# Optimization experiments

Measured on AMD Instinct MI355X. Metric: run time of the kernel, lower is better.

## Reference

```python
import jax, jax.numpy as jnp
import numpy as np

D_MODEL = 1024
N_HEADS = 16
D_K = D_MODEL // N_HEADS
THETA = 10000.0
B, S = 4, 2048


def _rope(x, positions):
    # x: [B, H, S, D_K]; positions: [S] int
    half = D_K // 2
    inv_freq = THETA ** (-jnp.arange(0, half, dtype=jnp.float32) * 2.0 / D_K)  # [half]
    ang = positions.astype(jnp.float32)[:, None] * inv_freq[None, :]  # [S, half]
    cos = jnp.cos(ang)[None, None, :, :]
    sin = jnp.sin(ang)[None, None, :, :]
    x_even = x[..., 0::2]
    x_odd = x[..., 1::2]
    out_even = x_even * cos - x_odd * sin
    out_odd = x_even * sin + x_odd * cos
    # interleave back to original layout
    out = jnp.stack([out_even, out_odd], axis=-1).reshape(x.shape)
    return out


def setup_inputs() -> dict:
    key = jax.random.key(0)
    ks = jax.random.split(key, 5)
    scale = 1.0 / np.sqrt(D_MODEL)
    return {
        "x": jax.random.normal(ks[0], (B, S, D_MODEL), dtype=jnp.float32),
        "token_positions": jnp.arange(S, dtype=jnp.int64 if jax.config.jax_enable_x64 else jnp.int32),
        "Wq": jax.random.normal(ks[1], (D_MODEL, D_MODEL), dtype=jnp.float32) * scale,
        "Wk": jax.random.normal(ks[2], (D_MODEL, D_MODEL), dtype=jnp.float32) * scale,
        "Wv": jax.random.normal(ks[3], (D_MODEL, D_MODEL), dtype=jnp.float32) * scale,
        "Wo": jax.random.normal(ks[4], (D_MODEL, D_MODEL), dtype=jnp.float32) * scale,
    }


def reference(x, token_positions, Wq, Wk, Wv, Wo):
    bsz, seq_len, _ = x.shape
    # projections (Linear_Transform: y = x @ W^T, no bias)
    def proj(W):
        h = jnp.einsum("bsd,ed->bse", x, W)
        return h.reshape(bsz, seq_len, N_HEADS, D_K).transpose(0, 2, 1, 3)  # [B,H,S,Dk]
    Q = proj(Wq)
    K = proj(Wk)
    V = proj(Wv)
    Q = _rope(Q, token_positions)
    K = _rope(K, token_positions)
    # scaled dot product attention with causal mask
    scores = jnp.einsum("bhqd,bhkd->bhqk", Q, K) / jnp.sqrt(jnp.float32(D_K))
    causal = jnp.tril(jnp.ones((seq_len, seq_len), dtype=bool))  # [S,S]
    scores = jnp.where(causal[None, None, :, :], scores, -jnp.inf)
    attn = jax.nn.softmax(scores, axis=-1)
    out = jnp.einsum("bhqk,bhkd->bhqd", attn, V)
    out = out.transpose(0, 2, 1, 3).reshape(bsz, seq_len, D_MODEL)
    return jnp.einsum("bsd,ed->bse", out, Wo)
```

## Files before the change

### kernel.cpp

```cpp
#include <hip/hip_runtime.h>
#include <hip/hip_bf16.h>
#include <cstdint>
#include <cstddef>

typedef __attribute__((ext_vector_type(4))) float f32x4;
typedef __attribute__((ext_vector_type(8))) short bf16x8;
typedef unsigned int u32;
typedef unsigned short u16;


__device__ __forceinline__ u16 f2bf(float x) {
  u32 u = __builtin_bit_cast(u32, x);
  u += 0x7fffu + ((u >> 16) & 1u);
  return (u16)(u >> 16);
}

__device__ __forceinline__ u32 cvt_pk_bf16(float lo, float hi) {
  u32 r;
  asm("v_cvt_pk_bf16_f32 %0, %1, %2" : "=v"(r) : "v"(lo), "v"(hi));
  return r;
}

__device__ __forceinline__ void gl_lds16(const void* g, void* l) {
  __builtin_amdgcn_global_load_lds(
      (const __attribute__((address_space(1))) u32*)(uintptr_t)g,
      (__attribute__((address_space(3))) u32*)(u32)(uintptr_t)l,
      16, 0, 0);
}

#define MFMA16(a, b, c) __builtin_amdgcn_mfma_f32_16x16x32_bf16((a), (b), (c), 0, 0, 0)


__global__ void cast_all_k(const float* __restrict__ x, const float* __restrict__ wq,
                           const float* __restrict__ wk, const float* __restrict__ wv,
                           const float* __restrict__ wo, u16* __restrict__ xb,
                           u16* __restrict__ wqb, u16* __restrict__ wkb,
                           u16* __restrict__ wvb, u16* __restrict__ wob) {
  int blk = blockIdx.x;
  const float* s; u16* d; int i;
  if (blk < 8192)       { s = x;  d = xb;  i = blk * 256; }
  else if (blk < 9216)  { s = wq; d = wqb; i = (blk - 8192) * 256; }
  else if (blk < 10240) { s = wk; d = wkb; i = (blk - 9216) * 256; }
  else if (blk < 11264) { s = wv; d = wvb; i = (blk - 10240) * 256; }
  else                  { s = wo; d = wob; i = (blk - 11264) * 256; }
  i += threadIdx.x;
  const float4 v = reinterpret_cast<const float4*>(s)[i];
  uint2 o;
  o.x = cvt_pk_bf16(v.x, v.y);
  o.y = cvt_pk_bf16(v.z, v.w);
  reinterpret_cast<uint2*>(d)[i] = o;
}


__global__ void rope_table_k(const int* __restrict__ pos, float2* __restrict__ cs) {
  int idx = blockIdx.x * 256 + threadIdx.x;
  int s = idx >> 5, i = idx & 31;
  float inv = powf(10000.0f, -(float)i * (1.0f / 32.0f));
  float ang = (float)pos[s] * inv;
  cs[idx] = float2{cosf(ang), sinf(ang)};
}


__global__ __launch_bounds__(256, 2)
void gemm_qkv(const u16* __restrict__ A, const u16* __restrict__ B,
              const float2* __restrict__ cs, u16* __restrict__ Qr,
              u16* __restrict__ Kr, u16* __restrict__ Vt, float qscale) {
  const int K = 1024;
  __shared__ u16 a_lds[2][128 * 32];
  __shared__ u16 b_lds[2][128 * 32];
  const int tid = threadIdx.x;
  const int l = tid & 63;
  const int w = tid >> 6;
  const int wm = w >> 1, wn = w & 1;
  const int bm = blockIdx.y, bn = blockIdx.x;

  const u16* Ab = A + (size_t)bm * 128 * K;
  const u16* Bb = B + (size_t)bn * 128 * K;

  auto stage = [&](int bq, int k0) {
#pragma unroll
    for (int half = 0; half < 2; ++half) {
      int t = half * 256 + tid;
      int row = t >> 2, slot = t & 3;
      int sp = slot ^ ((row >> 1) & 3);
      gl_lds16(Ab + (size_t)row * K + k0 + sp * 8, &a_lds[bq][t * 8]);
      gl_lds16(Bb + (size_t)row * K + k0 + sp * 8, &b_lds[bq][t * 8]);
    }
  };

  const f32x4 fz = {0.f, 0.f, 0.f, 0.f};
  f32x4 acc[4][4];
#pragma unroll
  for (int mi = 0; mi < 4; ++mi)
#pragma unroll
    for (int ni = 0; ni < 4; ++ni) acc[mi][ni] = fz;

  const int nk = K >> 5;
  stage(0, 0);
  int buf = 0;
  for (int kt = 0; kt < nk; ++kt) {
    __syncthreads();
    if (kt + 1 < nk) stage(buf ^ 1, (kt + 1) * 32);
    bf16x8 af[4], bf[4];
#pragma unroll
    for (int mi = 0; mi < 4; ++mi) {
      int row = wm * 64 + mi * 16 + (l & 15);
      int sp = (l >> 4) ^ ((row >> 1) & 3);
      af[mi] = *(const bf16x8*)&a_lds[buf][row * 32 + sp * 8];
    }
#pragma unroll
    for (int ni = 0; ni < 4; ++ni) {
      int row = wn * 64 + ni * 16 + (l & 15);
      int sp = (l >> 4) ^ ((row >> 1) & 3);
      bf[ni] = *(const bf16x8*)&b_lds[buf][row * 32 + sp * 8];
    }
#pragma unroll
    for (int mi = 0; mi < 4; ++mi)
#pragma unroll
      for (int ni = 0; ni < 4; ++ni)
        acc[mi][ni] = MFMA16(af[mi], bf[ni], acc[mi][ni]);
    buf ^= 1;
  }

  const int sector = bn >> 3;
  const int colb = ((bn & 7) << 7) + wn * 64;
  const int c = l & 15, h4 = l >> 4;

  if (sector == 2) {
#pragma unroll
    for (int mi = 0; mi < 4; ++mi) {
      int row = bm * 128 + wm * 64 + mi * 16 + 4 * h4;
      int b_ = row >> 11, s = row & 2047;
#pragma unroll
      for (int ni = 0; ni < 4; ++ni) {
        int cv = colb + ni * 16 + c;
        int hh = cv >> 6, dk = cv & 63;
        f32x4 v = acc[mi][ni];
        uint2 st;
        st.x = cvt_pk_bf16(v[0], v[1]);
        st.y = cvt_pk_bf16(v[2], v[3]);
        *(uint2*)&Vt[(((size_t)b_ * 16 + hh) << 17) + ((size_t)dk << 11) + s] = st;
      }
    }
  } else {
    u16* dst = sector ? Kr : Qr;
    const float scale = sector ? 1.0f : qscale;
#pragma unroll
    for (int mi = 0; mi < 4; ++mi) {
      int row0 = bm * 128 + wm * 64 + mi * 16 + 4 * h4;
#pragma unroll
      for (int ni = 0; ni < 4; ++ni) {
        int cv = colb + ni * 16 + c;
        int hh = cv >> 6, i2 = cv & 63;
        f32x4 v = acc[mi][ni];
        f32x4 pv;
#pragma unroll
        for (int j = 0; j < 4; ++j) pv[j] = __shfl_xor(v[j], 1);
        if (!(l & 1)) {
#pragma unroll
          for (int j = 0; j < 4; ++j) {
            int r = row0 + j, s = r & 2047, b_ = r >> 11;
            float2 t = cs[(s << 5) + (i2 >> 1)];
            float oe = (v[j] * t.x - pv[j] * t.y) * scale;
            float oo = (v[j] * t.y + pv[j] * t.x) * scale;
            *(u32*)&dst[(((size_t)(b_ * 16 + hh) * 2048 + s) << 6) + i2] =
                cvt_pk_bf16(oe, oo);
          }
        }
      }
    }
  }
}


__global__ __launch_bounds__(256, 2)
void gemm_bt(const u16* __restrict__ A, const u16* __restrict__ B,
             float* __restrict__ C, int M, int N, int K) {
  __shared__ u16 a_lds[2][128 * 32];
  __shared__ u16 b_lds[2][128 * 32];
  const int tid = threadIdx.x;
  const int l = tid & 63;
  const int w = tid >> 6;
  const int wm = w >> 1, wn = w & 1;
  const int bm = blockIdx.y, bn = blockIdx.x;

  const u16* Ab = A + (size_t)bm * 128 * K;
  const u16* Bb = B + (size_t)bn * 128 * K;

  auto stage = [&](int bq, int k0) {
#pragma unroll
    for (int half = 0; half < 2; ++half) {
      int t = half * 256 + tid;
      int row = t >> 2, slot = t & 3;
      int sp = slot ^ ((row >> 1) & 3);
      gl_lds16(Ab + (size_t)row * K + k0 + sp * 8, &a_lds[bq][t * 8]);
      gl_lds16(Bb + (size_t)row * K + k0 + sp * 8, &b_lds[bq][t * 8]);
    }
  };

  const f32x4 fz = {0.f, 0.f, 0.f, 0.f};
  f32x4 acc[4][4];
#pragma unroll
  for (int mi = 0; mi < 4; ++mi)
#pragma unroll
    for (int ni = 0; ni < 4; ++ni) acc[mi][ni] = fz;

  const int nk = K >> 5;
  stage(0, 0);
  int buf = 0;
  for (int kt = 0; kt < nk; ++kt) {
    __syncthreads();
    if (kt + 1 < nk) stage(buf ^ 1, (kt + 1) * 32);
    bf16x8 af[4], bf[4];
#pragma unroll
    for (int mi = 0; mi < 4; ++mi) {
      int row = wm * 64 + mi * 16 + (l & 15);
      int sp = (l >> 4) ^ ((row >> 1) & 3);
      af[mi] = *(const bf16x8*)&a_lds[buf][row * 32 + sp * 8];
    }
#pragma unroll
    for (int ni = 0; ni < 4; ++ni) {
      int row = wn * 64 + ni * 16 + (l & 15);
      int sp = (l >> 4) ^ ((row >> 1) & 3);
      bf[ni] = *(const bf16x8*)&b_lds[buf][row * 32 + sp * 8];
    }
#pragma unroll
    for (int mi = 0; mi < 4; ++mi)
#pragma unroll
      for (int ni = 0; ni < 4; ++ni)
        acc[mi][ni] = MFMA16(af[mi], bf[ni], acc[mi][ni]);
    buf ^= 1;
  }

#pragma unroll
  for (int mi = 0; mi < 4; ++mi) {
    int rbase = bm * 128 + wm * 64 + mi * 16 + ((l >> 4) << 2);
#pragma unroll
    for (int ni = 0; ni < 4; ++ni) {
      int col = bn * 128 + wn * 64 + ni * 16 + (l & 15);
      f32x4 v = acc[mi][ni];
#pragma unroll
      for (int j = 0; j < 4; ++j)
        C[(size_t)(rbase + j) * N + col] = v[j];
    }
  }
}


__global__ __launch_bounds__(256, 4)
void attn_k(const u16* __restrict__ Q, const u16* __restrict__ K,
            const u16* __restrict__ V, u16* __restrict__ O) {
  const int S = 2048;
  __shared__ u16 k_lds[2][64 * 64];
  __shared__ u16 v_lds[2][64 * 64];

  const int tid = threadIdx.x, l = tid & 63, w = tid >> 6;
  const int c = l & 15, h = l >> 4;

  const int wg = blockIdx.x;
  const int idx = (wg & 7) * 128 + (wg >> 3);
  const int bh = idx >> 4, pairI = idx & 15;

  const u16* Kb = K + (size_t)bh * S * 64;
  const u16* Vb = V + (size_t)bh * 64 * S;
  const int b = bh >> 4, hd = bh & 15;
  const f32x4 fz = {0.f, 0.f, 0.f, 0.f};

  int bperm[4];
#pragma unroll
  for (int tt = 0; tt < 4; ++tt)
    bperm[tt] = ((((l & 16) << 1) | ((tt >> 1) << 4) | c) << 2);

  auto stageKV = [&](int bq, int kv0) {
#pragma unroll
    for (int half = 0; half < 2; ++half) {
      int t = half * 256 + tid;
      int row = t >> 3, slot = t & 7;
      int sp = slot ^ (row & 7);
      gl_lds16(Kb + (size_t)(kv0 + row) * 64 + sp * 8, &k_lds[bq][t * 8]);
      gl_lds16(Vb + (size_t)row * S + kv0 + sp * 8, &v_lds[bq][t * 8]);
    }
  };

#pragma unroll 1
  for (int ph = 0; ph < 2; ++ph) {
    const int qi = ph ? (31 - pairI) : pairI;
    const int q0 = qi * 64;
    const int nkv = qi + 1;
    const u16* Qb = Q + ((size_t)bh * S + q0) * 64;

    bf16x8 qf[2];
#pragma unroll
    for (int ks = 0; ks < 2; ++ks)
      qf[ks] = *(const bf16x8*)(Qb + (size_t)(w * 16 + c) * 64 + ks * 32 + h * 8);
    __builtin_amdgcn_sched_barrier(0);
    stageKV(0, 0);

    f32x4 oacc[4];
#pragma unroll
    for (int ni = 0; ni < 4; ++ni) oacc[ni] = fz;
    float m_run = -1e30f, l_run = 0.f;

    int buf = 0;
#pragma unroll 1
    for (int t = 0; t < nkv; ++t) {
      if (t + 1 < nkv) {
        stageKV(buf ^ 1, (t + 1) * 64);
        __builtin_amdgcn_sched_barrier(0);
        asm volatile("s_waitcnt vmcnt(4)" ::: "memory");
      } else {
        asm volatile("s_waitcnt vmcnt(0)" ::: "memory");
      }
      __builtin_amdgcn_sched_barrier(0);
      __builtin_amdgcn_s_barrier();
      __builtin_amdgcn_sched_barrier(0);

      f32x4 sc[4];
#pragma unroll
      for (int kvb = 0; kvb < 4; ++kvb) sc[kvb] = fz;
      __builtin_amdgcn_s_setprio(1);
#pragma unroll
      for (int ks = 0; ks < 2; ++ks)
#pragma unroll
        for (int kvb = 0; kvb < 4; ++kvb) {
          int row = kvb * 16 + c;
          int sp = (4 * ks + h) ^ (row & 7);
          bf16x8 kf = *(const bf16x8*)&k_lds[buf][row * 64 + sp * 8];
          sc[kvb] = MFMA16(kf, qf[ks], sc[kvb]);
        }
      __builtin_amdgcn_s_setprio(0);

      if (t == qi) {
        int qg = q0 + w * 16 + c;
#pragma unroll
        for (int kvb = 0; kvb < 4; ++kvb)
#pragma unroll
          for (int j = 0; j < 4; ++j) {
            int kvg = t * 64 + kvb * 16 + 4 * h + j;
            if (kvg > qg) sc[kvb][j] = -1e30f;
          }
      }

      float mx = -1e30f;
#pragma unroll
      for (int kvb = 0; kvb < 4; ++kvb)
#pragma unroll
        for (int j = 0; j < 4; ++j) mx = fmaxf(mx, sc[kvb][j]);
      mx = fmaxf(mx, __shfl_xor(mx, 16));
      mx = fmaxf(mx, __shfl_xor(mx, 32));

      const bool norescale = __all(mx <= m_run);
      float mnew = norescale ? m_run : fmaxf(m_run, mx);
      float ps = 0.f;
#pragma unroll
      for (int kvb = 0; kvb < 4; ++kvb)
#pragma unroll
        for (int j = 0; j < 4; ++j) {
          float e = exp2f(sc[kvb][j] - mnew);
          sc[kvb][j] = e;
          ps += e;
        }
      ps += __shfl_xor(ps, 16);
      ps += __shfl_xor(ps, 32);

      if (norescale) {
        l_run += ps;
      } else {
        float alpha = exp2f(m_run - mnew);
        l_run = l_run * alpha + ps;
        m_run = mnew;
        float aj[4];
#pragma unroll
        for (int j = 0; j < 4; ++j) aj[j] = __shfl(alpha, 20 * h + j);
#pragma unroll
        for (int ni = 0; ni < 4; ++ni)
#pragma unroll
          for (int j = 0; j < 4; ++j) oacc[ni][j] *= aj[j];
      }

      u32 pk[4][2];
#pragma unroll
      for (int kvb = 0; kvb < 4; ++kvb) {
        pk[kvb][0] = cvt_pk_bf16(sc[kvb][0], sc[kvb][1]);
        pk[kvb][1] = cvt_pk_bf16(sc[kvb][2], sc[kvb][3]);
      }

#pragma unroll
      for (int ks = 0; ks < 2; ++ks) {
        union { u32 u[4]; bf16x8 v; } af;
#pragma unroll
        for (int tt = 0; tt < 4; ++tt) {
          u32 lo = (u32)__builtin_amdgcn_ds_bpermute(bperm[tt], (int)pk[2 * ks][tt & 1]);
          u32 hi = (u32)__builtin_amdgcn_ds_bpermute(bperm[tt], (int)pk[2 * ks + 1][tt & 1]);
          af.u[tt] = (l & 32) ? hi : lo;
        }
        __builtin_amdgcn_s_setprio(1);
#pragma unroll
        for (int ni = 0; ni < 4; ++ni) {
          int row = ni * 16 + c;
          int sp = (4 * ks + h) ^ (row & 7);
          bf16x8 vf = *(const bf16x8*)&v_lds[buf][row * 64 + sp * 8];
          oacc[ni] = MFMA16(af.v, vf, oacc[ni]);
        }
        __builtin_amdgcn_s_setprio(0);
      }

      __builtin_amdgcn_sched_barrier(0);
      __builtin_amdgcn_s_barrier();
      __builtin_amdgcn_sched_barrier(0);
      buf ^= 1;
    }

    float invl[4];
#pragma unroll
    for (int j = 0; j < 4; ++j)
      invl[j] = 1.f / __shfl(l_run, 20 * h + j);
#pragma unroll
    for (int ni = 0; ni < 4; ++ni)
#pragma unroll
      for (int j = 0; j < 4; ++j) {
        int srow = q0 + w * 16 + 4 * h + j;
        int dk = ni * 16 + c;
        O[((size_t)(b * 2048 + srow) << 10) + hd * 64 + dk] = f2bf(oacc[ni][j] * invl[j]);
      }
  }
}


extern "C" void kernel_launch(void* const* d_in, const int* in_sizes, int n_in,
                              void* d_out, int out_size, void* d_ws, size_t ws_size,
                              hipStream_t stream) {
  (void)in_sizes; (void)n_in; (void)out_size; (void)ws_size;
  const float* x  = (const float*)d_in[0];
  const int* pos  = (const int*)d_in[1];
  const float* Wq = (const float*)d_in[2];
  const float* Wk = (const float*)d_in[3];
  const float* Wv = (const float*)d_in[4];
  const float* Wo = (const float*)d_in[5];
  float* out = (float*)d_out;

  const int S = 2048, D = 1024;
  const size_t M = (size_t)4 * S;

  char* ws = (char*)d_ws;
  size_t off = 0;
  auto alloc = [&](size_t bytes) {
    void* p = ws + off;
    off += (bytes + 255) & ~(size_t)255;
    return p;
  };
  u16* xb   = (u16*)alloc(M * D * 2);
  u16* wqb  = (u16*)alloc((size_t)D * D * 2);
  u16* wkb  = (u16*)alloc((size_t)D * D * 2);
  u16* wvb  = (u16*)alloc((size_t)D * D * 2);
  u16* wob  = (u16*)alloc((size_t)D * D * 2);
  u16* Qr   = (u16*)alloc(M * D * 2);
  u16* Kr   = (u16*)alloc(M * D * 2);
  u16* Vt   = (u16*)alloc(M * D * 2);
  u16* Ob   = (u16*)alloc(M * D * 2);
  float2* csT = (float2*)alloc((size_t)S * 32 * 8);

  cast_all_k<<<12288, 256, 0, stream>>>(x, Wq, Wk, Wv, Wo, xb, wqb, wkb, wvb, wob);
  rope_table_k<<<(S * 32) / 256, 256, 0, stream>>>(pos, csT);

  const float QSCALE = 0.125f * 1.4426950408889634f;

  gemm_qkv<<<dim3(24, (unsigned)(M / 128)), 256, 0, stream>>>(
      xb, wqb, csT, Qr, Kr, Vt, QSCALE);
  attn_k<<<1024, 256, 0, stream>>>(Qr, Kr, Vt, Ob);
  gemm_bt<<<dim3(8, (unsigned)(M / 128)), 256, 0, stream>>>(Ob, wob, out, (int)M, D, D);
}
```

Baseline: 207.6 us.

## Double attention query tile per workgroup to reuse K/V LDS tiles

Each wave now handles 32 query rows instead of 16, so every workgroup processes a 128-row query block and reuses each staged K and V tile across two MFMA row groups. The grid is halved to 512 workgroups and the launch bound drops to 2 waves per SIMD to allow more registers. The causal masking now covers the last two KV tiles of each block. The aim is to cut LDS and global K/V traffic per query row. In exchange it raises register pressure, lowers occupancy and gives coarser load balance across CUs.

```diff
diff --git a/kernel.cpp b/kernel.cpp
--- a/kernel.cpp
+++ b/kernel.cpp
@@ -247,7 +247,7 @@
 }
 
 
-__global__ __launch_bounds__(256, 4)
+__global__ __launch_bounds__(256, 2)
 void attn_k(const u16* __restrict__ Q, const u16* __restrict__ K,
             const u16* __restrict__ V, u16* __restrict__ O) {
   const int S = 2048;
@@ -258,8 +258,8 @@
   const int c = l & 15, h = l >> 4;
 
   const int wg = blockIdx.x;
-  const int idx = (wg & 7) * 128 + (wg >> 3);
-  const int bh = idx >> 4, pairI = idx & 15;
+  const int idx = (wg & 7) * 64 + (wg >> 3);
+  const int bh = idx >> 3, pairI = idx & 7;
 
   const u16* Kb = K + (size_t)bh * S * 64;
   const u16* Vb = V + (size_t)bh * 64 * S;
@@ -284,22 +284,27 @@
 
 #pragma unroll 1
   for (int ph = 0; ph < 2; ++ph) {
-    const int qi = ph ? (31 - pairI) : pairI;
-    const int q0 = qi * 64;
-    const int nkv = qi + 1;
+    const int qi = ph ? (15 - pairI) : pairI;
+    const int q0 = qi * 128;
+    const int nkv = 2 * qi + 2;
     const u16* Qb = Q + ((size_t)bh * S + q0) * 64;
 
-    bf16x8 qf[2];
-#pragma unroll
-    for (int ks = 0; ks < 2; ++ks)
-      qf[ks] = *(const bf16x8*)(Qb + (size_t)(w * 16 + c) * 64 + ks * 32 + h * 8);
+    bf16x8 qf[2][2];
+#pragma unroll
+    for (int half = 0; half < 2; ++half)
+#pragma unroll
+      for (int ks = 0; ks < 2; ++ks)
+        qf[half][ks] = *(const bf16x8*)(
+            Qb + (size_t)(w * 32 + half * 16 + c) * 64 + ks * 32 + h * 8);
     __builtin_amdgcn_sched_barrier(0);
     stageKV(0, 0);
 
-    f32x4 oacc[4];
-#pragma unroll
-    for (int ni = 0; ni < 4; ++ni) oacc[ni] = fz;
-    float m_run = -1e30f, l_run = 0.f;
+    f32x4 oacc[2][4];
+#pragma unroll
+    for (int half = 0; half < 2; ++half)
+#pragma unroll
+      for (int ni = 0; ni < 4; ++ni) oacc[half][ni] = fz;
+    float m_run[2] = {-1e30f, -1e30f}, l_run[2] = {0.f, 0.f};
 
     int buf = 0;
 #pragma unroll 1
@@ -315,94 +320,121 @@
       __builtin_amdgcn_s_barrier();
       __builtin_amdgcn_sched_barrier(0);
 
-      f32x4 sc[4];
-#pragma unroll
-      for (int kvb = 0; kvb < 4; ++kvb) sc[kvb] = fz;
-      __builtin_amdgcn_s_setprio(1);
-#pragma unroll
-      for (int ks = 0; ks < 2; ++ks)
+      f32x4 sc[2][4];
+#pragma unroll
+      for (int half = 0; half < 2; ++half)
+#pragma unroll
+        for (int kvb = 0; kvb < 4; ++kvb) sc[half][kvb] = fz;
+#pragma unroll
+      for (int ks = 0; ks < 2; ++ks) {
+        bf16x8 kf[4];
 #pragma unroll
         for (int kvb = 0; kvb < 4; ++kvb) {
           int row = kvb * 16 + c;
           int sp = (4 * ks + h) ^ (row & 7);
-          bf16x8 kf = *(const bf16x8*)&k_lds[buf][row * 64 + sp * 8];
-          sc[kvb] = MFMA16(kf, qf[ks], sc[kvb]);
-        }
-      __builtin_amdgcn_s_setprio(0);
-
-      if (t == qi) {
-        int qg = q0 + w * 16 + c;
+          kf[kvb] = *(const bf16x8*)&k_lds[buf][row * 64 + sp * 8];
+        }
+        __builtin_amdgcn_s_setprio(1);
+#pragma unroll
+        for (int half = 0; half < 2; ++half)
+#pragma unroll
+          for (int kvb = 0; kvb < 4; ++kvb)
+            sc[half][kvb] = MFMA16(kf[kvb], qf[half][ks], sc[half][kvb]);
+        __builtin_amdgcn_s_setprio(0);
+      }
+
+      if (t >= nkv - 2) {
+#pragma unroll
+        for (int half = 0; half < 2; ++half) {
+          int qg = q0 + w * 32 + half * 16 + c;
+#pragma unroll
+          for (int kvb = 0; kvb < 4; ++kvb)
+#pragma unroll
+            for (int j = 0; j < 4; ++j) {
+              int kvg = t * 64 + kvb * 16 + 4 * h + j;
+              if (kvg > qg) sc[half][kvb][j] = -1e30f;
+            }
+        }
+      }
+
+      float mx[2];
+#pragma unroll
+      for (int half = 0; half < 2; ++half) {
+        float m = -1e30f;
 #pragma unroll
         for (int kvb = 0; kvb < 4; ++kvb)
 #pragma unroll
+          for (int j = 0; j < 4; ++j) m = fmaxf(m, sc[half][kvb][j]);
+        m = fmaxf(m, __shfl_xor(m, 16));
+        m = fmaxf(m, __shfl_xor(m, 32));
+        mx[half] = m;
+      }
+      const bool nores = __all((mx[0] <= m_run[0]) && (mx[1] <= m_run[1]));
+#pragma unroll
+      for (int half = 0; half < 2; ++half) {
+        float mnew = nores ? m_run[half] : fmaxf(m_run[half], mx[half]);
+        float ps = 0.f;
+#pragma unroll
+        for (int kvb = 0; kvb < 4; ++kvb)
+#pragma unroll
           for (int j = 0; j < 4; ++j) {
-            int kvg = t * 64 + kvb * 16 + 4 * h + j;
-            if (kvg > qg) sc[kvb][j] = -1e30f;
+            float e = exp2f(sc[half][kvb][j] - mnew);
+            sc[half][kvb][j] = e;
+            ps += e;
           }
-      }
-
-      float mx = -1e30f;
-#pragma unroll
-      for (int kvb = 0; kvb < 4; ++kvb)
-#pragma unroll
-        for (int j = 0; j < 4; ++j) mx = fmaxf(mx, sc[kvb][j]);
-      mx = fmaxf(mx, __shfl_xor(mx, 16));
-      mx = fmaxf(mx, __shfl_xor(mx, 32));
-
-      const bool norescale = __all(mx <= m_run);
-      float mnew = norescale ? m_run : fmaxf(m_run, mx);
-      float ps = 0.f;
-#pragma unroll
-      for (int kvb = 0; kvb < 4; ++kvb)
-#pragma unroll
-        for (int j = 0; j < 4; ++j) {
-          float e = exp2f(sc[kvb][j] - mnew);
-          sc[kvb][j] = e;
-          ps += e;
-        }
-      ps += __shfl_xor(ps, 16);
-      ps += __shfl_xor(ps, 32);
-
-      if (norescale) {
-        l_run += ps;
-      } else {
-        float alpha = exp2f(m_run - mnew);
-        l_run = l_run * alpha + ps;
-        m_run = mnew;
-        float aj[4];
-#pragma unroll
-        for (int j = 0; j < 4; ++j) aj[j] = __shfl(alpha, 20 * h + j);
-#pragma unroll
-        for (int ni = 0; ni < 4; ++ni)
-#pragma unroll
-          for (int j = 0; j < 4; ++j) oacc[ni][j] *= aj[j];
-      }
-
-      u32 pk[4][2];
-#pragma unroll
-      for (int kvb = 0; kvb < 4; ++kvb) {
-        pk[kvb][0] = cvt_pk_bf16(sc[kvb][0], sc[kvb][1]);
-        pk[kvb][1] = cvt_pk_bf16(sc[kvb][2], sc[kvb][3]);
-      }
+        ps += __shfl_xor(ps, 16);
+        ps += __shfl_xor(ps, 32);
+        if (nores) {
+          l_run[half] += ps;
+        } else {
+          float alpha = exp2f(m_run[half] - mnew);
+          l_run[half] = l_run[half] * alpha + ps;
+          m_run[half] = mnew;
+          float aj[4];
+#pragma unroll
+          for (int j = 0; j < 4; ++j) aj[j] = __shfl(alpha, 20 * h + j);
+#pragma unroll
+          for (int ni = 0; ni < 4; ++ni)
+#pragma unroll
+            for (int j = 0; j < 4; ++j) oacc[half][ni][j] *= aj[j];
+        }
+      }
+
+      u32 pk[2][4][2];
+#pragma unroll
+      for (int half = 0; half < 2; ++half)
+#pragma unroll
+        for (int kvb = 0; kvb < 4; ++kvb) {
+          pk[half][kvb][0] = cvt_pk_bf16(sc[half][kvb][0], sc[half][kvb][1]);
+          pk[half][kvb][1] = cvt_pk_bf16(sc[half][kvb][2], sc[half][kvb][3]);
+        }
 
 #pragma unroll
       for (int ks = 0; ks < 2; ++ks) {
-        union { u32 u[4]; bf16x8 v; } af;
-#pragma unroll
-        for (int tt = 0; tt < 4; ++tt) {
-          u32 lo = (u32)__builtin_amdgcn_ds_bpermute(bperm[tt], (int)pk[2 * ks][tt & 1]);
-          u32 hi = (u32)__builtin_amdgcn_ds_bpermute(bperm[tt], (int)pk[2 * ks + 1][tt & 1]);
-          af.u[tt] = (l & 32) ? hi : lo;
-        }
-        __builtin_amdgcn_s_setprio(1);
+        bf16x8 vf[4];
 #pragma unroll
         for (int ni = 0; ni < 4; ++ni) {
           int row = ni * 16 + c;
           int sp = (4 * ks + h) ^ (row & 7);
-          bf16x8 vf = *(const bf16x8*)&v_lds[buf][row * 64 + sp * 8];
-          oacc[ni] = MFMA16(af.v, vf, oacc[ni]);
-        }
-        __builtin_amdgcn_s_setprio(0);
+          vf[ni] = *(const bf16x8*)&v_lds[buf][row * 64 + sp * 8];
+        }
+#pragma unroll
+        for (int half = 0; half < 2; ++half) {
+          union { u32 u[4]; bf16x8 v; } af;
+#pragma unroll
+          for (int tt = 0; tt < 4; ++tt) {
+            u32 lo = (u32)__builtin_amdgcn_ds_bpermute(bperm[tt],
+                                                       (int)pk[half][2 * ks][tt & 1]);
+            u32 hi = (u32)__builtin_amdgcn_ds_bpermute(bperm[tt],
+                                                       (int)pk[half][2 * ks + 1][tt & 1]);
+            af.u[tt] = (l & 32) ? hi : lo;
+          }
+          __builtin_amdgcn_s_setprio(1);
+#pragma unroll
+          for (int ni = 0; ni < 4; ++ni)
+            oacc[half][ni] = MFMA16(af.v, vf[ni], oacc[half][ni]);
+          __builtin_amdgcn_s_setprio(0);
+        }
       }
 
       __builtin_amdgcn_sched_barrier(0);
@@ -411,18 +443,22 @@
       buf ^= 1;
     }
 
-    float invl[4];
-#pragma unroll
-    for (int j = 0; j < 4; ++j)
-      invl[j] = 1.f / __shfl(l_run, 20 * h + j);
-#pragma unroll
-    for (int ni = 0; ni < 4; ++ni)
-#pragma unroll
-      for (int j = 0; j < 4; ++j) {
-        int srow = q0 + w * 16 + 4 * h + j;
-        int dk = ni * 16 + c;
-        O[((size_t)(b * 2048 + srow) << 10) + hd * 64 + dk] = f2bf(oacc[ni][j] * invl[j]);
-      }
+#pragma unroll
+    for (int half = 0; half < 2; ++half) {
+      float invl[4];
+#pragma unroll
+      for (int j = 0; j < 4; ++j)
+        invl[j] = 1.f / __shfl(l_run[half], 20 * h + j);
+#pragma unroll
+      for (int ni = 0; ni < 4; ++ni)
+#pragma unroll
+        for (int j = 0; j < 4; ++j) {
+          int srow = q0 + w * 32 + half * 16 + 4 * h + j;
+          int dk = ni * 16 + c;
+          O[((size_t)(b * 2048 + srow) << 10) + hd * 64 + dk] =
+              f2bf(oacc[half][ni][j] * invl[j]);
+        }
+    }
   }
 }
 
@@ -467,6 +503,6 @@
 
   gemm_qkv<<<dim3(24, (unsigned)(M / 128)), 256, 0, stream>>>(
       xb, wqb, csT, Qr, Kr, Vt, QSCALE);
-  attn_k<<<1024, 256, 0, stream>>>(Qr, Kr, Vt, Ob);
+  attn_k<<<512, 256, 0, stream>>>(Qr, Kr, Vt, Ob);
   gemm_bt<<<dim3(8, (unsigned)(M / 128)), 256, 0, stream>>>(Ob, wob, out, (int)M, D, D);
 }
```

Measured after the change: 214.7 us. 1.03x slower.

## Switch attention to 32x32 MFMA tiles with 128-row query blocks

Applied to the files above, without the earlier changes.

Rewrites the attention inner loop to use 32x32x16 bf16 MFMA instructions, with each wave owning 32 query rows, so each workgroup handles 128 query rows and the grid halves to 512 blocks. The P-matrix relayout now uses v_permlane32_swap instead of ds_bpermute, and row statistics need only one cross-lane shuffle. The aim is to cut LDS traffic per FLOP and the shuffle and permute overhead. In exchange it uses more registers (launch bounds lowered to 2 waves per SIMD) and gives coarser causal load balance with fewer blocks.

```diff
diff --git a/kernel.cpp b/kernel.cpp
--- a/kernel.cpp
+++ b/kernel.cpp
@@ -4,6 +4,7 @@
 #include <cstddef>
 
 typedef __attribute__((ext_vector_type(4))) float f32x4;
+typedef __attribute__((ext_vector_type(16))) float f32x16;
 typedef __attribute__((ext_vector_type(8))) short bf16x8;
 typedef unsigned int u32;
 typedef unsigned short u16;
@@ -19,6 +20,10 @@
   u32 r;
   asm("v_cvt_pk_bf16_f32 %0, %1, %2" : "=v"(r) : "v"(lo), "v"(hi));
   return r;
+}
+
+__device__ __forceinline__ void perm_swap(u32& a, u32& b) {
+  asm("v_permlane32_swap_b32 %0, %1" : "+v"(a), "+v"(b));
 }
 
 __device__ __forceinline__ void gl_lds16(const void* g, void* l) {
@@ -29,6 +34,7 @@
 }
 
 #define MFMA16(a, b, c) __builtin_amdgcn_mfma_f32_16x16x32_bf16((a), (b), (c), 0, 0, 0)
+#define MFMA32(a, b, c) __builtin_amdgcn_mfma_f32_32x32x16_bf16((a), (b), (c), 0, 0, 0)
 
 
 __global__ void cast_all_k(const float* __restrict__ x, const float* __restrict__ wq,
@@ -247,7 +253,7 @@
 }
 
 
-__global__ __launch_bounds__(256, 4)
+__global__ __launch_bounds__(256, 2)
 void attn_k(const u16* __restrict__ Q, const u16* __restrict__ K,
             const u16* __restrict__ V, u16* __restrict__ O) {
   const int S = 2048;
@@ -255,21 +261,15 @@
   __shared__ u16 v_lds[2][64 * 64];
 
   const int tid = threadIdx.x, l = tid & 63, w = tid >> 6;
-  const int c = l & 15, h = l >> 4;
+  const int lane31 = l & 31, hi = l >> 5;
 
   const int wg = blockIdx.x;
-  const int idx = (wg & 7) * 128 + (wg >> 3);
-  const int bh = idx >> 4, pairI = idx & 15;
+  const int idx = (wg & 7) * 64 + (wg >> 3);
+  const int bh = idx >> 3, pairI = idx & 7;
 
   const u16* Kb = K + (size_t)bh * S * 64;
   const u16* Vb = V + (size_t)bh * 64 * S;
   const int b = bh >> 4, hd = bh & 15;
-  const f32x4 fz = {0.f, 0.f, 0.f, 0.f};
-
-  int bperm[4];
-#pragma unroll
-  for (int tt = 0; tt < 4; ++tt)
-    bperm[tt] = ((((l & 16) << 1) | ((tt >> 1) << 4) | c) << 2);
 
   auto stageKV = [&](int bq, int kv0) {
 #pragma unroll
@@ -284,21 +284,24 @@
 
 #pragma unroll 1
   for (int ph = 0; ph < 2; ++ph) {
-    const int qi = ph ? (31 - pairI) : pairI;
-    const int q0 = qi * 64;
-    const int nkv = qi + 1;
-    const u16* Qb = Q + ((size_t)bh * S + q0) * 64;
-
-    bf16x8 qf[2];
-#pragma unroll
-    for (int ks = 0; ks < 2; ++ks)
-      qf[ks] = *(const bf16x8*)(Qb + (size_t)(w * 16 + c) * 64 + ks * 32 + h * 8);
+    const int qi = ph ? (15 - pairI) : pairI;
+    const int q0 = qi * 128;
+    const int nkv = 2 * qi + 2;
+    const int qrow = q0 + w * 32 + lane31;
+    const u16* Qp = Q + ((size_t)bh * S + qrow) * 64;
+
+    bf16x8 qf[4];
+#pragma unroll
+    for (int ks = 0; ks < 4; ++ks)
+      qf[ks] = *(const bf16x8*)(Qp + ks * 16 + hi * 8);
     __builtin_amdgcn_sched_barrier(0);
     stageKV(0, 0);
 
-    f32x4 oacc[4];
-#pragma unroll
-    for (int ni = 0; ni < 4; ++ni) oacc[ni] = fz;
+    f32x16 oacc[2];
+#pragma unroll
+    for (int dt = 0; dt < 2; ++dt)
+#pragma unroll
+      for (int r = 0; r < 16; ++r) oacc[dt][r] = 0.f;
     float m_run = -1e30f, l_run = 0.f;
 
     int buf = 0;
@@ -315,95 +318,93 @@
       __builtin_amdgcn_s_barrier();
       __builtin_amdgcn_sched_barrier(0);
 
-      f32x4 sc[4];
-#pragma unroll
-      for (int kvb = 0; kvb < 4; ++kvb) sc[kvb] = fz;
+      f32x16 sc[2];
+#pragma unroll
+      for (int dt = 0; dt < 2; ++dt)
+#pragma unroll
+        for (int r = 0; r < 16; ++r) sc[dt][r] = 0.f;
       __builtin_amdgcn_s_setprio(1);
 #pragma unroll
-      for (int ks = 0; ks < 2; ++ks)
-#pragma unroll
-        for (int kvb = 0; kvb < 4; ++kvb) {
-          int row = kvb * 16 + c;
-          int sp = (4 * ks + h) ^ (row & 7);
-          bf16x8 kf = *(const bf16x8*)&k_lds[buf][row * 64 + sp * 8];
-          sc[kvb] = MFMA16(kf, qf[ks], sc[kvb]);
+      for (int ks = 0; ks < 4; ++ks) {
+        int sp = (2 * ks + hi) ^ (lane31 & 7);
+#pragma unroll
+        for (int dt = 0; dt < 2; ++dt) {
+          bf16x8 kf = *(const bf16x8*)&k_lds[buf][(dt * 32 + lane31) * 64 + sp * 8];
+          sc[dt] = MFMA32(kf, qf[ks], sc[dt]);
         }
+      }
       __builtin_amdgcn_s_setprio(0);
 
-      if (t == qi) {
-        int qg = q0 + w * 16 + c;
-#pragma unroll
-        for (int kvb = 0; kvb < 4; ++kvb)
-#pragma unroll
-          for (int j = 0; j < 4; ++j) {
-            int kvg = t * 64 + kvb * 16 + 4 * h + j;
-            if (kvg > qg) sc[kvb][j] = -1e30f;
+      bf16x8 vf[2][4];
+#pragma unroll
+      for (int ks = 0; ks < 4; ++ks) {
+        int sp = (2 * ks + hi) ^ (lane31 & 7);
+#pragma unroll
+        for (int dt = 0; dt < 2; ++dt)
+          vf[dt][ks] = *(const bf16x8*)&v_lds[buf][(dt * 32 + lane31) * 64 + sp * 8];
+      }
+
+      if (t >= nkv - 2) {
+#pragma unroll
+        for (int dt = 0; dt < 2; ++dt)
+#pragma unroll
+          for (int r = 0; r < 16; ++r) {
+            int kvg = t * 64 + dt * 32 + (r & 3) + 8 * (r >> 2) + 4 * hi;
+            if (kvg > qrow) sc[dt][r] = -1e30f;
           }
       }
 
       float mx = -1e30f;
 #pragma unroll
-      for (int kvb = 0; kvb < 4; ++kvb)
-#pragma unroll
-        for (int j = 0; j < 4; ++j) mx = fmaxf(mx, sc[kvb][j]);
-      mx = fmaxf(mx, __shfl_xor(mx, 16));
+      for (int dt = 0; dt < 2; ++dt)
+#pragma unroll
+        for (int r = 0; r < 16; ++r) mx = fmaxf(mx, sc[dt][r]);
       mx = fmaxf(mx, __shfl_xor(mx, 32));
 
-      const bool norescale = __all(mx <= m_run);
-      float mnew = norescale ? m_run : fmaxf(m_run, mx);
+      const bool nores = __all(mx <= m_run);
+      float mnew = nores ? m_run : fmaxf(m_run, mx);
       float ps = 0.f;
 #pragma unroll
-      for (int kvb = 0; kvb < 4; ++kvb)
-#pragma unroll
-        for (int j = 0; j < 4; ++j) {
-          float e = exp2f(sc[kvb][j] - mnew);
-          sc[kvb][j] = e;
+      for (int dt = 0; dt < 2; ++dt)
+#pragma unroll
+        for (int r = 0; r < 16; ++r) {
+          float e = exp2f(sc[dt][r] - mnew);
+          sc[dt][r] = e;
           ps += e;
         }
-      ps += __shfl_xor(ps, 16);
       ps += __shfl_xor(ps, 32);
-
-      if (norescale) {
+      if (nores) {
         l_run += ps;
       } else {
         float alpha = exp2f(m_run - mnew);
         l_run = l_run * alpha + ps;
         m_run = mnew;
-        float aj[4];
-#pragma unroll
-        for (int j = 0; j < 4; ++j) aj[j] = __shfl(alpha, 20 * h + j);
-#pragma unroll
-        for (int ni = 0; ni < 4; ++ni)
-#pragma unroll
-          for (int j = 0; j < 4; ++j) oacc[ni][j] *= aj[j];
-      }
-
-      u32 pk[4][2];
-#pragma unroll
-      for (int kvb = 0; kvb < 4; ++kvb) {
-        pk[kvb][0] = cvt_pk_bf16(sc[kvb][0], sc[kvb][1]);
-        pk[kvb][1] = cvt_pk_bf16(sc[kvb][2], sc[kvb][3]);
-      }
-
-#pragma unroll
-      for (int ks = 0; ks < 2; ++ks) {
-        union { u32 u[4]; bf16x8 v; } af;
-#pragma unroll
-        for (int tt = 0; tt < 4; ++tt) {
-          u32 lo = (u32)__builtin_amdgcn_ds_bpermute(bperm[tt], (int)pk[2 * ks][tt & 1]);
-          u32 hi = (u32)__builtin_amdgcn_ds_bpermute(bperm[tt], (int)pk[2 * ks + 1][tt & 1]);
-          af.u[tt] = (l & 32) ? hi : lo;
-        }
-        __builtin_amdgcn_s_setprio(1);
-#pragma unroll
-        for (int ni = 0; ni < 4; ++ni) {
-          int row = ni * 16 + c;
-          int sp = (4 * ks + h) ^ (row & 7);
-          bf16x8 vf = *(const bf16x8*)&v_lds[buf][row * 64 + sp * 8];
-          oacc[ni] = MFMA16(af.v, vf, oacc[ni]);
-        }
-        __builtin_amdgcn_s_setprio(0);
-      }
+#pragma unroll
+        for (int dt = 0; dt < 2; ++dt)
+#pragma unroll
+          for (int r = 0; r < 16; ++r) oacc[dt][r] *= alpha;
+      }
+
+      union { u32 u[4]; bf16x8 v; } pf[4];
+#pragma unroll
+      for (int ks = 0; ks < 4; ++ks) {
+        const int sidx = ks >> 1, rb = (ks & 1) * 8;
+        u32 c01 = cvt_pk_bf16(sc[sidx][rb + 0], sc[sidx][rb + 1]);
+        u32 c23 = cvt_pk_bf16(sc[sidx][rb + 2], sc[sidx][rb + 3]);
+        u32 c45 = cvt_pk_bf16(sc[sidx][rb + 4], sc[sidx][rb + 5]);
+        u32 c67 = cvt_pk_bf16(sc[sidx][rb + 6], sc[sidx][rb + 7]);
+        perm_swap(c01, c45);
+        perm_swap(c23, c67);
+        pf[ks].u[0] = c01; pf[ks].u[1] = c23; pf[ks].u[2] = c45; pf[ks].u[3] = c67;
+      }
+
+      __builtin_amdgcn_s_setprio(1);
+#pragma unroll
+      for (int dt = 0; dt < 2; ++dt)
+#pragma unroll
+        for (int ks = 0; ks < 4; ++ks)
+          oacc[dt] = MFMA32(vf[dt][ks], pf[ks].v, oacc[dt]);
+      __builtin_amdgcn_s_setprio(0);
 
       __builtin_amdgcn_sched_barrier(0);
       __builtin_amdgcn_s_barrier();
@@ -411,17 +412,16 @@
       buf ^= 1;
     }
 
-    float invl[4];
-#pragma unroll
-    for (int j = 0; j < 4; ++j)
-      invl[j] = 1.f / __shfl(l_run, 20 * h + j);
-#pragma unroll
-    for (int ni = 0; ni < 4; ++ni)
-#pragma unroll
-      for (int j = 0; j < 4; ++j) {
-        int srow = q0 + w * 16 + 4 * h + j;
-        int dk = ni * 16 + c;
-        O[((size_t)(b * 2048 + srow) << 10) + hd * 64 + dk] = f2bf(oacc[ni][j] * invl[j]);
+    float inv = 1.f / l_run;
+    u16* Ob = O + (((size_t)(b * 2048 + qrow)) << 10) + hd * 64;
+#pragma unroll
+    for (int dt = 0; dt < 2; ++dt)
+#pragma unroll
+      for (int g = 0; g < 4; ++g) {
+        uint2 st;
+        st.x = cvt_pk_bf16(oacc[dt][4 * g + 0] * inv, oacc[dt][4 * g + 1] * inv);
+        st.y = cvt_pk_bf16(oacc[dt][4 * g + 2] * inv, oacc[dt][4 * g + 3] * inv);
+        *(uint2*)&Ob[dt * 32 + g * 8 + hi * 4] = st;
       }
   }
 }
@@ -467,6 +467,6 @@
 
   gemm_qkv<<<dim3(24, (unsigned)(M / 128)), 256, 0, stream>>>(
       xb, wqb, csT, Qr, Kr, Vt, QSCALE);
-  attn_k<<<1024, 256, 0, stream>>>(Qr, Kr, Vt, Ob);
+  attn_k<<<512, 256, 0, stream>>>(Qr, Kr, Vt, Ob);
   gemm_bt<<<dim3(8, (unsigned)(M / 128)), 256, 0, stream>>>(Ob, wob, out, (int)M, D, D);
 }
```

Measured after the change: 197.1 us. 5.1% less time.
